# Optimization experiments

Hardware: AMD Instinct MI355X
Metric: run time of the kernel (lower is better)

Reference implementation:

```python
import jax, jax.numpy as jnp
import numpy as np

B_BOXES = 5
N_CLASSES = 80
LAMBDA_COORD = 5.0
LAMBDA_NOOBJ = 0.5
LAMBDA_CLASS = 1.0
EPS = 1e-6


def _corners(b):
    # b: (..., 4) center-format (x, y, w, h) -> x1, y1, x2, y2
    x, y, w, h = b[..., 0], b[..., 1], b[..., 2], b[..., 3]
    return x - w / 2, y - h / 2, x + w / 2, y + h / 2


def pairwise_iou(p_box, t_box):
    # p_box, t_box: (N, S, S, B, 4) -> ious: (N, S, S, B_pred, B_tgt)
    px1, py1, px2, py2 = _corners(p_box[..., :, None, :])
    tx1, ty1, tx2, ty2 = _corners(t_box[..., None, :, :])
    iw = jnp.clip(jnp.minimum(px2, tx2) - jnp.maximum(px1, tx1), 0.0)
    ih = jnp.clip(jnp.minimum(py2, ty2) - jnp.maximum(py1, ty1), 0.0)
    inter = iw * ih
    area_p = (px2 - px1) * (py2 - py1)
    area_t = (tx2 - tx1) * (ty2 - ty1)
    return inter / (area_p + area_t - inter + EPS)


def setup_inputs() -> dict:
    key = jax.random.key(0)
    k1, k2 = jax.random.split(key)
    N, S = 128, 26
    ch = B_BOXES * (5 + N_CLASSES)  # 425
    preds = jax.random.normal(k1, (N, S, S, ch), dtype=jnp.float32)
    targets = jax.random.normal(k2, (N, S, S, ch), dtype=jnp.float32)
    return {"preds": preds, "targets": targets}


def reference(preds, targets):
    N, S = preds.shape[0], preds.shape[1]
    D = 5 + N_CLASSES
    p = preds.reshape(N, S, S, B_BOXES, D)
    t = targets.reshape(N, S, S, B_BOXES, D)

    ious = pairwise_iou(p[..., :4], t[..., :4])          # (N,S,S,B,B)
    best = jnp.argmax(ious, axis=-1)                      # (N,S,S,B)
    idx = jnp.broadcast_to(best[..., None], t.shape)
    matched = jnp.take_along_axis(t, idx, axis=3)         # (N,S,S,B,D)

    obj = (matched[..., 4] > 0).astype(p.dtype)           # (N,S,S,B)
    noobj = 1.0 - obj

    xy_loss = LAMBDA_COORD * jnp.sum(obj[..., None] * (p[..., 0:2] - matched[..., 0:2]) ** 2)

    pwh = jnp.sqrt(jnp.abs(p[..., 2:4] + EPS))
    twh = jnp.sqrt(jnp.abs(matched[..., 2:4] + EPS))
    wh_loss = LAMBDA_COORD * jnp.sum(obj[..., None] * (pwh - twh) ** 2)

    conf_sq = (p[..., 4] - matched[..., 4]) ** 2
    conf_loss_obj = jnp.sum(obj * conf_sq)
    conf_loss_noobj = LAMBDA_NOOBJ * jnp.sum(noobj * conf_sq)

    tcls = jnp.argmax(t[..., 5:], axis=-1)                # (N,S,S,B)
    logp = jax.nn.log_softmax(p[..., 5:], axis=-1)
    nll = -jnp.take_along_axis(logp, tcls[..., None], axis=-1)[..., 0]
    class_loss = LAMBDA_CLASS * jnp.sum(obj * nll)

    return xy_loss + wh_loss + conf_loss_obj + conf_loss_noobj + class_loss
```

## Files before the change

kernel.cpp:

```cpp
#include <hip/hip_runtime.h>
#include <math.h>

#define NB 5
#define NC 80
#define DD 85
#define CH 425
#define EPSF 1e-6f
#define CPB 16
#define CHUNK_F (CPB * CH)
#define CHUNK_F4 (CHUNK_F / 4)
#define TPB 256
#define NITER 7

__global__ __launch_bounds__(TPB) void yolo_loss_kernel(
    const float* __restrict__ preds,
    const float* __restrict__ targets,
    float* __restrict__ out)
{
    __shared__ float4 s_p4[CHUNK_F4];
    __shared__ float4 s_t4[CHUNK_F4];
    __shared__ float s_wsum[4];
    const float* sp = (const float*)s_p4;
    const float* st = (const float*)s_t4;

    const int tid = threadIdx.x;
    const long long g0 = (long long)blockIdx.x * CHUNK_F;
    const float4* gp = (const float4*)(preds + g0);
    const float4* gt = (const float4*)(targets + g0);

    float4 rp[NITER], rt[NITER];
    #pragma unroll
    for (int j = 0; j < NITER; ++j) {
        const int idx = tid + j * TPB;
        if (idx < CHUNK_F4) { rp[j] = gp[idx]; rt[j] = gt[idx]; }
    }
    #pragma unroll
    for (int j = 0; j < NITER; ++j) {
        const int idx = tid + j * TPB;
        if (idx < CHUNK_F4) { s_p4[idx] = rp[j]; s_t4[idx] = rt[j]; }
    }
    __syncthreads();

    float acc = 0.0f;
    if (tid < 2 * CPB * NB) {
        const int t = tid >> 1;
        const int h = tid & 1;
        const int kb = t * DD + 5 + h * 40;
        float s  = 0.0f;
        float bv = -INFINITY;
        int   bi = 0x7fffffff;
        float bp = 0.0f;
        #pragma unroll 8
        for (int k = 0; k < 40; ++k) {
            const float pl = sp[kb + k];
            const float tl = st[kb + k];
            s += __expf(pl);
            if (tl > bv) { bv = tl; bi = h * 40 + k; bp = pl; }
        }
        s += __shfl_xor(s, 1, 64);
        const float ov = __shfl_xor(bv, 1, 64);
        const int   oi = __shfl_xor(bi, 1, 64);
        const float op = __shfl_xor(bp, 1, 64);
        if (ov > bv || (ov == bv && oi < bi)) { bv = ov; bi = oi; bp = op; }
        const float nll = __logf(s) - bp;

        if (h == 0) {
            const int c = t / 5;
            const int pb = t * DD;
            const float px = sp[pb + 0], py = sp[pb + 1], pw = sp[pb + 2],
                        ph = sp[pb + 3], pconf = sp[pb + 4];
            const float px1 = px - pw * 0.5f, py1 = py - ph * 0.5f;
            const float px2 = px + pw * 0.5f, py2 = py + ph * 0.5f;
            const float area_p = (px2 - px1) * (py2 - py1);

            float best = -INFINITY;
            float mx = 0.f, my = 0.f, mw = 0.f, mh = 0.f, mconf = 0.f;
            #pragma unroll
            for (int j = 0; j < NB; ++j) {
                const int tb = c * CH + j * DD;
                const float tx = st[tb + 0], ty = st[tb + 1], tw = st[tb + 2],
                            th = st[tb + 3], tcf = st[tb + 4];
                const float tx1 = tx - tw * 0.5f, ty1 = ty - th * 0.5f;
                const float tx2 = tx + tw * 0.5f, ty2 = ty + th * 0.5f;
                float iw = fminf(px2, tx2) - fmaxf(px1, tx1); iw = fmaxf(iw, 0.0f);
                float ih = fminf(py2, ty2) - fmaxf(py1, ty1); ih = fmaxf(ih, 0.0f);
                const float inter  = iw * ih;
                const float area_t = (tx2 - tx1) * (ty2 - ty1);
                const float iou    = inter / (area_p + area_t - inter + EPSF);
                if (iou > best) { best = iou; mx = tx; my = ty; mw = tw; mh = th; mconf = tcf; }
            }

            const float obj = (mconf > 0.0f) ? 1.0f : 0.0f;
            const float dx = px - mx, dy = py - my;
            float term = 5.0f * obj * (dx * dx + dy * dy);
            const float dw = sqrtf(fabsf(pw + EPSF)) - sqrtf(fabsf(mw + EPSF));
            const float dh = sqrtf(fabsf(ph + EPSF)) - sqrtf(fabsf(mh + EPSF));
            term += 5.0f * obj * (dw * dw + dh * dh);
            const float dc  = pconf - mconf;
            const float csq = dc * dc;
            term += obj * csq + 0.5f * (1.0f - obj) * csq;
            term += obj * nll;
            acc = term;
        }
    }

    #pragma unroll
    for (int off = 32; off > 0; off >>= 1) acc += __shfl_down(acc, off, 64);
    if ((tid & 63) == 0) s_wsum[tid >> 6] = acc;
    __syncthreads();
    if (tid == 0) {
        atomicAdd(out, s_wsum[0] + s_wsum[1] + s_wsum[2] + s_wsum[3]);
    }
}

extern "C" void kernel_launch(void* const* d_in, const int* in_sizes, int n_in,
                              void* d_out, int out_size, void* d_ws, size_t ws_size,
                              hipStream_t stream) {
    const float* preds   = (const float*)d_in[0];
    const float* targets = (const float*)d_in[1];
    float* out = (float*)d_out;

    const int ncells = in_sizes[0] / CH;
    const int blocks = ncells / CPB;

    hipMemsetAsync(out, 0, sizeof(float), stream);
    yolo_loss_kernel<<<blocks, TPB, 0, stream>>>(preds, targets, out);
}
```

Before: 368.0 us.

## Load tiles directly to LDS, halve cells per block, replace atomics with two-pass reduce

Global-to-shared staging now uses global_load_lds, so data no longer passes through registers. Cells per block drop from 16 to 8, which doubles the block count and shrinks LDS use for better occupancy. The class softmax work is split across four lanes per box instead of two, merged with xor shuffles. Per-block partial sums go to a workspace array and a second small kernel reduces them, replacing the memset and global atomic. The extra launch adds a little fixed overhead.

```diff
diff --git a/kernel.cpp b/kernel.cpp
--- a/kernel.cpp
+++ b/kernel.cpp
@@ -6,69 +6,82 @@
 #define DD 85
 #define CH 425
 #define EPSF 1e-6f
-#define CPB 16
+#define CPB 8
+#define TASKS (CPB * NB)
 #define CHUNK_F (CPB * CH)
 #define CHUNK_F4 (CHUNK_F / 4)
 #define TPB 256
-#define NITER 7
+#define NK ((CHUNK_F4 + TPB - 1) / TPB)
+
+__device__ __forceinline__ void gload_lds16(const float* g, float* l) {
+    __builtin_amdgcn_global_load_lds(
+        (const __attribute__((address_space(1))) void*)g,
+        (__attribute__((address_space(3))) void*)l,
+        16, 0, 0);
+}
 
 __global__ __launch_bounds__(TPB) void yolo_loss_kernel(
     const float* __restrict__ preds,
     const float* __restrict__ targets,
-    float* __restrict__ out)
+    float* __restrict__ partials,
+    int use_atomic)
 {
-    __shared__ float4 s_p4[CHUNK_F4];
-    __shared__ float4 s_t4[CHUNK_F4];
+    __shared__ __align__(16) float s_p[CHUNK_F];
+    __shared__ __align__(16) float s_t[CHUNK_F];
     __shared__ float s_wsum[4];
-    const float* sp = (const float*)s_p4;
-    const float* st = (const float*)s_t4;
 
-    const int tid = threadIdx.x;
-    const long long g0 = (long long)blockIdx.x * CHUNK_F;
-    const float4* gp = (const float4*)(preds + g0);
-    const float4* gt = (const float4*)(targets + g0);
+    const int tid  = threadIdx.x;
+    const int wave = tid >> 6;
+    const int lane = tid & 63;
 
-    float4 rp[NITER], rt[NITER];
+    const float* gp = preds   + (size_t)blockIdx.x * CHUNK_F;
+    const float* gt = targets + (size_t)blockIdx.x * CHUNK_F;
+
     #pragma unroll
-    for (int j = 0; j < NITER; ++j) {
-        const int idx = tid + j * TPB;
-        if (idx < CHUNK_F4) { rp[j] = gp[idx]; rt[j] = gt[idx]; }
+    for (int k = 0; k < NK; ++k) {
+        const int base = k * TPB + wave * 64;
+        const int idx  = base + lane;
+        if (idx < CHUNK_F4) {
+            gload_lds16(gp + 4 * (size_t)idx, s_p + 4 * base);
+            gload_lds16(gt + 4 * (size_t)idx, s_t + 4 * base);
+        }
     }
-    #pragma unroll
-    for (int j = 0; j < NITER; ++j) {
-        const int idx = tid + j * TPB;
-        if (idx < CHUNK_F4) { s_p4[idx] = rp[j]; s_t4[idx] = rt[j]; }
-    }
+    asm volatile("s_waitcnt vmcnt(0)" ::: "memory");
     __syncthreads();
 
     float acc = 0.0f;
-    if (tid < 2 * CPB * NB) {
-        const int t = tid >> 1;
-        const int h = tid & 1;
-        const int kb = t * DD + 5 + h * 40;
+    if (tid < 4 * TASKS) {
+        const int t = tid >> 2;
+        const int q = tid & 3;
+        const int kb = t * DD + 5 + q * 20;
+
         float s  = 0.0f;
         float bv = -INFINITY;
         int   bi = 0x7fffffff;
         float bp = 0.0f;
-        #pragma unroll 8
-        for (int k = 0; k < 40; ++k) {
-            const float pl = sp[kb + k];
-            const float tl = st[kb + k];
+        #pragma unroll 5
+        for (int k = 0; k < 20; ++k) {
+            const float pl = s_p[kb + k];
+            const float tl = s_t[kb + k];
             s += __expf(pl);
-            if (tl > bv) { bv = tl; bi = h * 40 + k; bp = pl; }
+            if (tl > bv) { bv = tl; bi = q * 20 + k; bp = pl; }
         }
-        s += __shfl_xor(s, 1, 64);
-        const float ov = __shfl_xor(bv, 1, 64);
-        const int   oi = __shfl_xor(bi, 1, 64);
-        const float op = __shfl_xor(bp, 1, 64);
-        if (ov > bv || (ov == bv && oi < bi)) { bv = ov; bi = oi; bp = op; }
-        const float nll = __logf(s) - bp;
+        #pragma unroll
+        for (int m = 1; m < 4; m <<= 1) {
+            s += __shfl_xor(s, m, 64);
+            const float ov = __shfl_xor(bv, m, 64);
+            const int   oi = __shfl_xor(bi, m, 64);
+            const float op = __shfl_xor(bp, m, 64);
+            if (ov > bv || (ov == bv && oi < bi)) { bv = ov; bi = oi; bp = op; }
+        }
 
-        if (h == 0) {
-            const int c = t / 5;
+        if (q == 0) {
+            const float nll = __logf(s) - bp;
+
+            const int c  = t / 5;
             const int pb = t * DD;
-            const float px = sp[pb + 0], py = sp[pb + 1], pw = sp[pb + 2],
-                        ph = sp[pb + 3], pconf = sp[pb + 4];
+            const float px = s_p[pb + 0], py = s_p[pb + 1], pw = s_p[pb + 2],
+                        ph = s_p[pb + 3], pconf = s_p[pb + 4];
             const float px1 = px - pw * 0.5f, py1 = py - ph * 0.5f;
             const float px2 = px + pw * 0.5f, py2 = py + ph * 0.5f;
             const float area_p = (px2 - px1) * (py2 - py1);
@@ -77,9 +90,9 @@
             float mx = 0.f, my = 0.f, mw = 0.f, mh = 0.f, mconf = 0.f;
             #pragma unroll
             for (int j = 0; j < NB; ++j) {
-                const int tb = c * CH + j * DD;
-                const float tx = st[tb + 0], ty = st[tb + 1], tw = st[tb + 2],
-                            th = st[tb + 3], tcf = st[tb + 4];
+                const int tb = (c * NB + j) * DD;
+                const float tx = s_t[tb + 0], ty = s_t[tb + 1], tw = s_t[tb + 2],
+                            th = s_t[tb + 3], tcf = s_t[tb + 4];
                 const float tx1 = tx - tw * 0.5f, ty1 = ty - th * 0.5f;
                 const float tx2 = tx + tw * 0.5f, ty2 = ty + th * 0.5f;
                 float iw = fminf(px2, tx2) - fmaxf(px1, tx1); iw = fmaxf(iw, 0.0f);
@@ -109,8 +122,23 @@
     if ((tid & 63) == 0) s_wsum[tid >> 6] = acc;
     __syncthreads();
     if (tid == 0) {
-        atomicAdd(out, s_wsum[0] + s_wsum[1] + s_wsum[2] + s_wsum[3]);
+        const float v = s_wsum[0] + s_wsum[1] + s_wsum[2] + s_wsum[3];
+        if (use_atomic) atomicAdd(partials, v);
+        else            partials[blockIdx.x] = v;
     }
+}
+
+__global__ __launch_bounds__(TPB) void reduce_kernel(
+    const float* __restrict__ partials, float* __restrict__ out, int n)
+{
+    float s = 0.0f;
+    for (int i = threadIdx.x; i < n; i += TPB) s += partials[i];
+    #pragma unroll
+    for (int off = 32; off > 0; off >>= 1) s += __shfl_down(s, off, 64);
+    __shared__ float wsum[4];
+    if ((threadIdx.x & 63) == 0) wsum[threadIdx.x >> 6] = s;
+    __syncthreads();
+    if (threadIdx.x == 0) out[0] = wsum[0] + wsum[1] + wsum[2] + wsum[3];
 }
 
 extern "C" void kernel_launch(void* const* d_in, const int* in_sizes, int n_in,
@@ -123,6 +151,12 @@
     const int ncells = in_sizes[0] / CH;
     const int blocks = ncells / CPB;
 
-    hipMemsetAsync(out, 0, sizeof(float), stream);
-    yolo_loss_kernel<<<blocks, TPB, 0, stream>>>(preds, targets, out);
+    if (ws_size >= (size_t)blocks * sizeof(float)) {
+        float* ws = (float*)d_ws;
+        yolo_loss_kernel<<<blocks, TPB, 0, stream>>>(preds, targets, ws, 0);
+        reduce_kernel<<<1, TPB, 0, stream>>>(ws, out, blocks);
+    } else {
+        hipMemsetAsync(out, 0, sizeof(float), stream);
+        yolo_loss_kernel<<<blocks, TPB, 0, stream>>>(preds, targets, out, 1);
+    }
 }
```

Measured after the change: 310.4 us. -15.6%, faster.
